# Optimization experiments

Hardware: AMD Instinct MI355X
Metric: run time of the kernel (lower is better)

## Reference

```python
import jax, jax.numpy as jnp
import numpy as np

T, B = 32, 64
H, W = 16, 16
FEAT = 32
CNN_DIM = 512
N_ACT = 5
MAP_OUT = FEAT * H * W  # 8192, flattened map readout


def _conv_relu(x, w, b, stride):
    y = jax.lax.conv_general_dilated(
        x, w, (stride, stride), 'VALID',
        dimension_numbers=('NCHW', 'OIHW', 'NCHW'))
    return jax.nn.relu(y + b[None, :, None, None])


def _mlp(x, w1, b1, w2, b2):
    return jax.nn.relu(x @ w1 + b1) @ w2 + b2


def setup_inputs() -> dict:
    key = jax.random.key(0)
    ks = jax.random.split(key, 32)
    g = lambda k, shape, fan: jax.random.normal(k, shape, jnp.float32) * (1.0 / np.sqrt(fan))
    inp = {}
    inp['image'] = jax.random.uniform(ks[0], (T * B, 84, 84, 3), jnp.float32) * 255.0
    inp['done'] = jnp.zeros((T, B), jnp.float32)
    inp['state0'] = jnp.zeros((B, FEAT, H, W), jnp.float32)
    inp['position'] = jax.random.randint(ks[1], (T * B, 2), 0, H).astype(jnp.int32)
    # NatureCNN params
    inp['w1'] = g(ks[2], (32, 3, 8, 8), 3 * 8 * 8); inp['b1'] = jnp.zeros((32,), jnp.float32)
    inp['w2'] = g(ks[3], (64, 32, 4, 4), 32 * 4 * 4); inp['b2'] = jnp.zeros((64,), jnp.float32)
    inp['w3'] = g(ks[4], (64, 64, 3, 3), 64 * 3 * 3); inp['b3'] = jnp.zeros((64,), jnp.float32)
    inp['wfc'] = g(ks[5], (64 * 7 * 7, CNN_DIM), 64 * 7 * 7); inp['bfc'] = jnp.zeros((CNN_DIM,), jnp.float32)
    # Map write projection
    inp['Ww'] = g(ks[6], (CNN_DIM, FEAT), CNN_DIM); inp['bw'] = jnp.zeros((FEAT,), jnp.float32)
    # pos_net MLP: one-hot(16)+one-hot(16)=32 -> 64
    inp['wp1'] = g(ks[7], (2 * H, 64), 2 * H); inp['bp1'] = jnp.zeros((64,), jnp.float32)
    inp['wp2'] = g(ks[8], (64, 64), 64); inp['bp2'] = jnp.zeros((64,), jnp.float32)
    # policy MLP: (MAP_OUT+64) -> 64 -> N_ACT
    inp['wpo1'] = g(ks[9], (MAP_OUT + 64, 64), MAP_OUT + 64); inp['bpo1'] = jnp.zeros((64,), jnp.float32)
    inp['wpo2'] = g(ks[10], (64, N_ACT), 64) * 0.01; inp['bpo2'] = jnp.zeros((N_ACT,), jnp.float32)
    # value MLP
    inp['wv1'] = g(ks[11], (MAP_OUT + 64, 64), MAP_OUT + 64); inp['bv1'] = jnp.zeros((64,), jnp.float32)
    inp['wv2'] = g(ks[12], (64, 1), 64); inp['bv2'] = jnp.zeros((1,), jnp.float32)
    return inp


def reference(image, done, state0, w1, b1, w2, b2, w3, b3, wfc, bfc, Ww, bw,
              wp1, bp1, wp2, bp2, wpo1, bpo1, wpo2, bpo2, wv1, bv1, wv2, bv2,
              position):
    # preprocess_image: /255 and NHWC -> NCHW
    x = jnp.transpose(image / 255.0, (0, 3, 1, 2))
    x = _conv_relu(x, w1, b1, 4)   # [TB,32,20,20]
    x = _conv_relu(x, w2, b2, 2)   # [TB,64,9,9]
    x = _conv_relu(x, w3, b3, 1)   # [TB,64,7,7]
    h = jax.nn.relu(x.reshape(x.shape[0], -1) @ wfc + bfc)  # [TB,512]

    h_seq = h.reshape(T, B, CNN_DIM)
    idx_seq = position.reshape(T, B, 2)
    benv = jnp.arange(B)

    def step(state, inp):
        h_t, d_t, i_t = inp
        masked = (1.0 - d_t)[:, None, None, None] * state  # reset done envs
        wfeat = h_t @ Ww + bw                              # [B,FEAT]
        state = masked.at[benv, :, i_t[:, 0], i_t[:, 1]].add(wfeat)
        return state, state.reshape(B, -1)                 # per-step map readout

    state, outs = jax.lax.scan(step, state0, (h_seq, done, idx_seq))
    hidden = outs.reshape(T * B, MAP_OUT)

    # position net on one-hot coords
    pos_oh = jnp.concatenate([jax.nn.one_hot(position[:, 0], H, dtype=hidden.dtype),
                              jax.nn.one_hot(position[:, 1], W, dtype=hidden.dtype)], axis=1)
    pos_feat = _mlp(pos_oh, wp1, bp1, wp2, bp2)            # [TB,64]
    hidden = jnp.concatenate([hidden, pos_feat], axis=1)

    logits = _mlp(hidden, wpo1, bpo1, wpo2, bpo2)          # [TB,N_ACT]
    v = _mlp(hidden, wv1, bv1, wv2, bv2)                   # [TB,1]
    return logits, v, state
```

## Files before the change

### kernel.cpp

```cpp
#include <hip/hip_runtime.h>
#include <hip/hip_bf16.h>


#define TT 32
#define BB 64
#define TBR 2048

typedef _Float16 half_t;
typedef __attribute__((ext_vector_type(4))) _Float16 half4;
typedef __attribute__((ext_vector_type(8))) _Float16 half8;
typedef __attribute__((ext_vector_type(4))) float f32x4;

#define OFF_W1T   0u
#define OFF_W2T   6144u
#define OFF_W3T   22528u
#define OFF_WF    40960u
#define OFF_PF    106496u
#define OFF_Y0    237568u
#define OFF_PP    245760u
#define OFF_H     507904u
#define OFF_DELTA 1556480u
#define OFF_WFCT  1818624u
#define OFF_C3    2621440u
#define OFF_H1    5832704u

__global__ __launch_bounds__(256) void prep_all(
    const float* __restrict__ w1, const float* __restrict__ w2,
    const float* __restrict__ w3, half_t* __restrict__ w1p,
    half_t* __restrict__ w2T, half_t* __restrict__ w3T,
    const float* __restrict__ wfc, half_t* __restrict__ wfcT) {
  __shared__ float t[32][33];
  int bx = blockIdx.x;
  if (bx < 304) {
    int g = bx * 256 + threadIdx.x;
    if (g < 8192) {
      int kk = g & 31, oc = (g >> 5) & 31, tap = g >> 10;
      half_t v = (half_t)0.f;
      if (kk < 24) {
        int kx = kk / 3, c = kk - 3 * kx;
        v = (half_t)(w1[oc * 192 + c * 64 + tap * 8 + kx] * (1.0f / 255.0f));
      }
      w1p[g] = v;
      return;
    }
    int g2 = g - 8192;
    if (g2 < 32768) {
      int c = g2 & 31, oc = (g2 >> 5) & 63, tap = g2 >> 11;
      w2T[g2] = (half_t)w2[oc * 512 + c * 16 + tap];
      return;
    }
    int g3 = g2 - 32768;
    if (g3 < 36864) {
      int c = g3 & 63, oc = (g3 >> 6) & 63, tap = g3 >> 12;
      w3T[g3] = (half_t)w3[oc * 576 + c * 9 + tap];
    }
    return;
  }
  int gb = bx - 304;
  int k0 = (gb % 98) * 32, n0 = (gb / 98) * 32;
  int tx = threadIdx.x & 31, ty = threadIdx.x >> 5;
#pragma unroll
  for (int i = 0; i < 4; ++i)
    t[ty + 8 * i][tx] = wfc[(size_t)(k0 + ty + 8 * i) * 512 + n0 + tx];
  __syncthreads();
#pragma unroll
  for (int i = 0; i < 4; ++i)
    wfcT[(size_t)(n0 + ty + 8 * i) * 3136 + k0 + tx] =
        (half_t)t[tx][ty + 8 * i];
}

#define C1_BANDF 5040
#define C1_BANDV 1260
#define C1OUT_OFF 10368
#define C1A(ip, bp)                                                     \
  (C1OUT_OFF + ((ip) >> 1) * 128 +                                      \
   (((((ip) & 1) << 6) | ((bp) & 0x30)) ^ ((((ip) >> 1) & 7) << 4)) +   \
   ((bp) & 15))
#define C2A(ir, bp) \
  ((ir) * 128 + (((bp) & 0x70) ^ (((ir) & 7) << 4)) + ((bp) & 15))
__global__ __launch_bounds__(256) void conv123_mfma(
    const float* __restrict__ img, const half_t* __restrict__ w1p,
    const float* __restrict__ b1, const half_t* __restrict__ w2T,
    const float* __restrict__ b2, const half_t* __restrict__ w3T,
    const float* __restrict__ b3, half_t* __restrict__ out) {
  __shared__ __align__(16) char lds[35968];
  half_t* stag = (half_t*)lds;
  int tid = threadIdx.x;
  int li = blockIdx.x;
  int w = tid >> 6, l = tid & 63, lc = l & 15, q = l >> 4;
  const float* ib = img + (size_t)li * 21168;

  half8 bfrag1[8][2];
#pragma unroll
  for (int tap = 0; tap < 8; ++tap)
#pragma unroll
    for (int t = 0; t < 2; ++t)
      bfrag1[tap][t] =
          *(const half8*)(w1p + (size_t)(tap * 32 + t * 16 + lc) * 32 + q * 8);
  float b1v[2] = {b1[lc], b1[16 + lc]};

  f32x4 fr[5];
#define C1_LOADB(b)                                                   \
  {                                                                   \
    const float* src = ib + 4032 * (b);                               \
    _Pragma("unroll") for (int i = 0; i < 5; ++i) {                   \
      int g = tid + 256 * i;                                          \
      if (g < C1_BANDV) fr[i] = *(const f32x4*)(src + 4 * g);         \
    }                                                                 \
  }
#define C1_WRITEB()                                                   \
  {                                                                   \
    _Pragma("unroll") for (int i = 0; i < 5; ++i) {                   \
      int g = tid + 256 * i;                                          \
      if (g < C1_BANDV) {                                             \
        half4 o;                                                      \
        _Pragma("unroll") for (int j = 0; j < 4; ++j)                 \
            o[j] = (half_t)fr[i][j];                                  \
        *(half4*)&stag[4 * g] = o;                                    \
      }                                                               \
    }                                                                 \
  }

  C1_LOADB(0);
  C1_WRITEB();
  __syncthreads();
  for (int b = 0; b < 5; ++b) {
    if (b < 4) C1_LOADB(b + 1);
    for (int tile = w; tile < 5; tile += 4) {
      int lp = tile * 16 + lc;
      int oyl = lp / 20, ox = lp - oyl * 20;
      f32x4 acc[2];
      acc[0] = (f32x4){0.f, 0.f, 0.f, 0.f};
      acc[1] = (f32x4){0.f, 0.f, 0.f, 0.f};
#pragma unroll
      for (int ky = 0; ky < 8; ++ky) {
        half8 af;
        if (q < 3) {
          const half_t* p = &stag[(4 * oyl + ky) * 252 + 12 * ox + q * 8];
          *(half4*)&af = *(const half4*)p;
          *((half4*)&af + 1) = *((const half4*)(p + 4));
        } else {
#pragma unroll
          for (int j = 0; j < 8; ++j) af[j] = (half_t)0.f;
        }
        acc[0] = __builtin_amdgcn_mfma_f32_16x16x32_f16(af, bfrag1[ky][0],
                                                        acc[0], 0, 0, 0);
        acc[1] = __builtin_amdgcn_mfma_f32_16x16x32_f16(af, bfrag1[ky][1],
                                                        acc[1], 0, 0, 0);
      }
#pragma unroll
      for (int t = 0; t < 2; ++t) {
#pragma unroll
        for (int r = 0; r < 4; ++r) {
          int ip = b * 80 + tile * 16 + q * 4 + r;
          int ch = t * 16 + lc;
          *(half_t*)(lds + C1A(ip, 2 * ch)) =
              (half_t)fmaxf(acc[t][r] + b1v[t], 0.f);
        }
      }
    }
    __syncthreads();
    if (b < 4) {
      C1_WRITEB();
      __syncthreads();
    }
  }

  {
    half8 bfrag2[16][2];
#pragma unroll
    for (int tap = 0; tap < 16; ++tap)
#pragma unroll
      for (int j = 0; j < 2; ++j) {
        int nt = (w & 1) * 2 + j;
        bfrag2[tap][j] = *(const half8*)(
            w2T + (size_t)(tap * 64 + nt * 16 + lc) * 32 + q * 8);
      }
    float b2v[2];
#pragma unroll
    for (int j = 0; j < 2; ++j) b2v[j] = b2[(w & 1) * 32 + j * 16 + lc];

#pragma unroll
    for (int ti = 0; ti < 3; ++ti) {
      int tile = (w >> 1) + 2 * ti;
      int row16 = tile * 16 + lc;
      int orow = row16 < 81 ? row16 : 80;
      int oy = orow / 9, ox = orow - oy * 9;
      f32x4 acc[2];
      acc[0] = (f32x4){0.f, 0.f, 0.f, 0.f};
      acc[1] = (f32x4){0.f, 0.f, 0.f, 0.f};
#pragma unroll
      for (int tap = 0; tap < 16; ++tap) {
        int ky = tap >> 2, kx = tap & 3;
        int ip = (2 * oy + ky) * 20 + 2 * ox + kx;
        half8 af = *(const half8*)(lds + C1A(ip, q * 16));
        acc[0] = __builtin_amdgcn_mfma_f32_16x16x32_f16(af, bfrag2[tap][0],
                                                        acc[0], 0, 0, 0);
        acc[1] = __builtin_amdgcn_mfma_f32_16x16x32_f16(af, bfrag2[tap][1],
                                                        acc[1], 0, 0, 0);
      }
#pragma unroll
      for (int j = 0; j < 2; ++j) {
#pragma unroll
        for (int r = 0; r < 4; ++r) {
          int mr = tile * 16 + q * 4 + r;
          if (mr < 81) {
            int col = (w & 1) * 32 + j * 16 + lc;
            *(half_t*)(lds + C2A(mr, 2 * col)) =
                (half_t)fmaxf(acc[j][r] + b2v[j], 0.f);
          }
        }
      }
    }
  }
  __syncthreads();

  {
    half8 bfrag3[9][2];
#pragma unroll
    for (int tap = 0; tap < 9; ++tap)
#pragma unroll
      for (int ch = 0; ch < 2; ++ch)
        bfrag3[tap][ch] = *(const half8*)(
            w3T + (size_t)(tap * 64 + w * 16 + lc) * 64 + ch * 32 + q * 8);
    float b3v = b3[w * 16 + lc];

    half_t* ob = out + (size_t)li * 3136;
#pragma unroll
    for (int tile = 0; tile < 4; ++tile) {
      int row16 = tile * 16 + lc;
      int orow = row16 < 49 ? row16 : 48;
      int oy = orow / 7, ox = orow - oy * 7;
      f32x4 acc = (f32x4){0.f, 0.f, 0.f, 0.f};
#pragma unroll
      for (int tap = 0; tap < 9; ++tap) {
        int ky = tap / 3, kx = tap - ky * 3;
        int ir = (oy + ky) * 9 + ox + kx;
#pragma unroll
        for (int ch = 0; ch < 2; ++ch) {
          half8 af = *(const half8*)(lds + C2A(ir, ch * 64 + q * 16));
          acc = __builtin_amdgcn_mfma_f32_16x16x32_f16(af, bfrag3[tap][ch],
                                                       acc, 0, 0, 0);
        }
      }
#pragma unroll
      for (int r = 0; r < 4; ++r) {
        int pos = tile * 16 + q * 4 + r;
        if (pos < 49) {
          int col = w * 16 + lc;
          ob[(size_t)col * 49 + pos] = (half_t)fmaxf(acc[r] + b3v, 0.f);
        }
      }
    }
  }
}

__global__ __launch_bounds__(256) void fc_mfma(
    const half_t* __restrict__ A, const half_t* __restrict__ Bt,
    float* __restrict__ h0, float* __restrict__ h1) {
  __shared__ __align__(16) half_t As[2][64 * 40];
  __shared__ __align__(16) half_t Bs[2][64 * 40];
  int tid = threadIdx.x;
  int m0 = blockIdx.y * 64, n0 = blockIdx.x * 64;
  int kh = blockIdx.z;
  int w = tid >> 6;
  int l = tid & 63;
  int lc = l & 15, q = l >> 4;
  int srow = tid >> 2, sseg = tid & 3;

  const half_t* aPtr = A + (size_t)(m0 + srow) * 3136 + kh * 1568 + sseg * 8;
  const half_t* bPtr = Bt + (size_t)(n0 + srow) * 3136 + kh * 1568 + sseg * 8;
  uint4 aReg = *(const uint4*)aPtr;
  uint4 bReg = *(const uint4*)bPtr;

  f32x4 acc[4];
#pragma unroll
  for (int t = 0; t < 4; ++t) acc[t] = (f32x4){0.f, 0.f, 0.f, 0.f};

  for (int s = 0; s < 49; ++s) {
    int cur = s & 1;
    *(uint4*)&As[cur][srow * 40 + sseg * 8] = aReg;
    *(uint4*)&Bs[cur][srow * 40 + sseg * 8] = bReg;
    __syncthreads();
    if (s < 48) {
      aReg = *(const uint4*)(aPtr + (s + 1) * 32);
      bReg = *(const uint4*)(bPtr + (s + 1) * 32);
    }
    half8 af = *(const half8*)&As[cur][(w * 16 + lc) * 40 + q * 8];
#pragma unroll
    for (int t = 0; t < 4; ++t) {
      half8 bf = *(const half8*)&Bs[cur][(t * 16 + lc) * 40 + q * 8];
      acc[t] = __builtin_amdgcn_mfma_f32_16x16x32_f16(af, bf, acc[t], 0, 0, 0);
    }
  }
  float* H = kh ? h1 : h0;
#pragma unroll
  for (int t = 0; t < 4; ++t) {
#pragma unroll
    for (int r = 0; r < 4; ++r) {
      int row = m0 + w * 16 + q * 4 + r;
      int col = n0 + t * 16 + lc;
      H[(size_t)row * 512 + col] = acc[t][r];
    }
  }
}

__global__ __launch_bounds__(256) void mid1_kernel(
    const float* __restrict__ h0, const float* __restrict__ h1,
    const float* __restrict__ bfc, const float* __restrict__ Ww,
    const float* __restrict__ bw, float* __restrict__ wf,
    const int* __restrict__ pos, const float* __restrict__ wp1,
    const float* __restrict__ bp1, const float* __restrict__ wp2,
    const float* __restrict__ bp2, float* __restrict__ pf,
    const float* __restrict__ s0, const float* __restrict__ wpo1,
    const float* __restrict__ wv1, float* __restrict__ y0) {
  __shared__ float red[128];
  int bx = blockIdx.x;
  if (bx < 256) {
    int g = bx * 256 + threadIdx.x;
    int row = g >> 5, oc = g & 31;
    float acc = bw[oc];
    const float* hr0 = h0 + (size_t)row * 512;
    const float* hr1 = h1 + (size_t)row * 512;
#pragma unroll 8
    for (int k = 0; k < 512; ++k)
      acc += fmaxf(hr0[k] + hr1[k] + bfc[k], 0.f) * Ww[k * 32 + oc];
    wf[g] = acc;
    return;
  }
  if (bx < 768) {
    int row = ((bx - 256) * 256 + threadIdx.x) >> 6;
    int l = threadIdx.x & 63;
    int p0 = pos[row * 2], p1 = pos[row * 2 + 1];
    float t1 = fmaxf(wp1[p0 * 64 + l] + wp1[(16 + p1) * 64 + l] + bp1[l], 0.f);
    float acc = bp2[l];
#pragma unroll
    for (int k = 0; k < 64; ++k) acc += __shfl(t1, k) * wp2[k * 64 + l];
    pf[row * 64 + l] = acc;
    return;
  }
  int g = bx - 768;
  int b = g >> 5, kc = g & 31;
  int n = threadIdx.x & 127, kh = threadIdx.x >> 7;
  const float* W = (n < 64) ? (wpo1 + n) : (wv1 + (n - 64));
  int k0 = kc * 256 + kh * 128;
  const float* s = s0 + (size_t)b * 8192 + k0;
  float acc = 0.f;
#pragma unroll 8
  for (int j = 0; j < 128; ++j) acc += s[j] * W[(size_t)(k0 + j) * 64];
  if (kh) red[n] = acc;
  __syncthreads();
  if (!kh) atomicAdd(y0 + b * 128 + n, acc + red[n]);
}

__global__ __launch_bounds__(256) void mid2_kernel(
    const int* __restrict__ pos, const float* __restrict__ wf,
    const float* __restrict__ wpo1, const float* __restrict__ wv1,
    float* __restrict__ delta, const float* __restrict__ s0,
    const float* __restrict__ done, float* __restrict__ out_state,
    const float* __restrict__ pf, float* __restrict__ pp) {
  int bx = blockIdx.x;
  if (bx < 1024) {
    int row = bx * 2 + (threadIdx.x >> 7);
    int n = threadIdx.x & 127;
    const float* W = (n < 64) ? (wpo1 + n) : (wv1 + (n - 64));
    int off = pos[row * 2] * 16 + pos[row * 2 + 1];
    const float* wfr = wf + row * 32;
    float d = 0.f;
#pragma unroll
    for (int c = 0; c < 32; ++c) d += wfr[c] * W[(size_t)(c * 256 + off) * 64];
    delta[(size_t)row * 128 + n] = d;
    return;
  }
  if (bx < 1088) {
    int b = bx - 1024, tid = threadIdx.x;
    float s[32];
#pragma unroll
    for (int c = 0; c < 32; ++c) s[c] = s0[(size_t)b * 8192 + c * 256 + tid];
    for (int t = 0; t < TT; ++t) {
      int row = t * BB + b;
      float mask = 1.f - done[row];
      int off = pos[row * 2] * 16 + pos[row * 2 + 1];
#pragma unroll
      for (int c = 0; c < 32; ++c) s[c] *= mask;
      if (tid == off) {
#pragma unroll
        for (int c = 0; c < 32; ++c) s[c] += wf[row * 32 + c];
      }
    }
#pragma unroll
    for (int c = 0; c < 32; ++c)
      out_state[(size_t)b * 8192 + c * 256 + tid] = s[c];
    return;
  }
  int row = (bx - 1088) * 2 + (threadIdx.x >> 7);
  int n = threadIdx.x & 127;
  const float* W = (n < 64) ? (wpo1 + n) : (wv1 + (n - 64));
  const float* pfr = pf + row * 64;
  float acc = 0.f;
#pragma unroll
  for (int k = 0; k < 64; ++k) acc += pfr[k] * W[(size_t)(8192 + k) * 64];
  pp[(size_t)row * 128 + n] = acc;
}

__global__ __launch_bounds__(128) void scan_head_kernel(
    const float* __restrict__ y0, const float* __restrict__ done,
    const float* __restrict__ delta, const float* __restrict__ pp,
    const float* __restrict__ bpo1, const float* __restrict__ bv1,
    const float* __restrict__ wpo2, const float* __restrict__ bpo2,
    const float* __restrict__ wv2, const float* __restrict__ bv2,
    float* __restrict__ logits, float* __restrict__ vout) {
  int b = blockIdx.x;
  int n = threadIdx.x;
  int l = n & 63, wv = n >> 6;
  float bias1 = wv ? bv1[l] : bpo1[l];
  float w2v[5];
  if (!wv) {
#pragma unroll
    for (int a = 0; a < 5; ++a) w2v[a] = wpo2[l * 5 + a];
  } else {
    w2v[0] = wv2[l];
  }
  float y = y0[b * 128 + n];
  for (int t = 0; t < TT; ++t) {
    int row = t * BB + b;
    y = y * (1.f - done[row]) + delta[(size_t)row * 128 + n];
    float act = fmaxf(y + pp[(size_t)row * 128 + n] + bias1, 0.f);
    if (!wv) {
#pragma unroll
      for (int a = 0; a < 5; ++a) {
        float pa = act * w2v[a];
#pragma unroll
        for (int m = 32; m >= 1; m >>= 1) pa += __shfl_xor(pa, m);
        if (l == 0) logits[row * 5 + a] = pa + bpo2[a];
      }
    } else {
      float pv = act * w2v[0];
#pragma unroll
      for (int m = 32; m >= 1; m >>= 1) pv += __shfl_xor(pv, m);
      if (l == 0) vout[row] = pv + bv2[0];
    }
  }
}

extern "C" void kernel_launch(void* const* d_in, const int* in_sizes, int n_in,
                              void* d_out, int out_size, void* d_ws, size_t ws_size,
                              hipStream_t stream) {
  const float* image = (const float*)d_in[0];
  const float* done = (const float*)d_in[1];
  const float* state0 = (const float*)d_in[2];
  const int* position = (const int*)d_in[3];
  const float* w1 = (const float*)d_in[4];
  const float* b1 = (const float*)d_in[5];
  const float* w2 = (const float*)d_in[6];
  const float* b2 = (const float*)d_in[7];
  const float* w3 = (const float*)d_in[8];
  const float* b3 = (const float*)d_in[9];
  const float* wfc = (const float*)d_in[10];
  const float* bfc = (const float*)d_in[11];
  const float* Ww = (const float*)d_in[12];
  const float* bw = (const float*)d_in[13];
  const float* wp1 = (const float*)d_in[14];
  const float* bp1 = (const float*)d_in[15];
  const float* wp2 = (const float*)d_in[16];
  const float* bp2 = (const float*)d_in[17];
  const float* wpo1 = (const float*)d_in[18];
  const float* bpo1 = (const float*)d_in[19];
  const float* wpo2 = (const float*)d_in[20];
  const float* bpo2 = (const float*)d_in[21];
  const float* wv1 = (const float*)d_in[22];
  const float* bv1 = (const float*)d_in[23];
  const float* wv2 = (const float*)d_in[24];
  const float* bv2 = (const float*)d_in[25];

  float* ws = (float*)d_ws;
  half_t* w1p = (half_t*)(ws + OFF_W1T);
  half_t* w2T = (half_t*)(ws + OFF_W2T);
  half_t* w3T = (half_t*)(ws + OFF_W3T);
  float* wf = ws + OFF_WF;
  float* pfb = ws + OFF_PF;
  float* y0 = ws + OFF_Y0;
  float* ppb = ws + OFF_PP;
  float* h0b = ws + OFF_H;
  float* h1b = ws + OFF_H1;
  float* deltab = ws + OFF_DELTA;
  half_t* wfcT = (half_t*)(ws + OFF_WFCT);
  half_t* c3b = (half_t*)(ws + OFF_C3);

  float* out = (float*)d_out;
  float* out_logits = out;
  float* out_v = out + 10240;
  float* out_state = out + 12288;

  hipMemsetAsync(y0, 0, 8192 * sizeof(float), stream);
  prep_all<<<1872, 256, 0, stream>>>(w1, w2, w3, w1p, w2T, w3T, wfc, wfcT);
  conv123_mfma<<<TBR, 256, 0, stream>>>(image, w1p, b1, w2T, b2, w3T, b3, c3b);
  fc_mfma<<<dim3(8, 32, 2), 256, 0, stream>>>(c3b, wfcT, h0b, h1b);
  mid1_kernel<<<2816, 256, 0, stream>>>(h0b, h1b, bfc, Ww, bw, wf, position,
                                        wp1, bp1, wp2, bp2, pfb, state0,
                                        wpo1, wv1, y0);
  mid2_kernel<<<2112, 256, 0, stream>>>(position, wf, wpo1, wv1, deltab,
                                        state0, done, out_state, pfb, ppb);
  scan_head_kernel<<<64, 128, 0, stream>>>(y0, done, deltab, ppb, bpo1, bv1,
                                           wpo2, bpo2, wv2, bv2,
                                           out_logits, out_v);
}
```

Baseline: 451.8 us.

## Enlarge FC GEMM tiles to 128x128 and split K four ways

The FC MFMA GEMM now computes 128x128 output tiles per block, with each wave holding a 2x8 grid of 16x16 accumulators, up from 64x64. The K dimension is split into four chunks instead of two, giving 256 blocks, and mid1 sums four partial outputs. The larger tiles raise operand reuse from LDS and cut global reloads of A and B. In exchange the blocks use more registers and LDS, and two extra partial buffers must be written and read back.

New measurement: 449.8 us. No clear change (-0.4%).

```diff
diff --git a/kernel.cpp b/kernel.cpp
--- a/kernel.cpp
+++ b/kernel.cpp
@@ -23,6 +23,8 @@
 #define OFF_WFCT  1818624u
 #define OFF_C3    2621440u
 #define OFF_H1    5832704u
+#define OFF_H2    6881280u
+#define OFF_H3    7929856u
 
 __global__ __launch_bounds__(256) void prep_all(
     const float* __restrict__ w1, const float* __restrict__ w2,
@@ -245,10 +247,10 @@
       }
 #pragma unroll
       for (int r = 0; r < 4; ++r) {
-        int pos = tile * 16 + q * 4 + r;
-        if (pos < 49) {
+        int pos2 = tile * 16 + q * 4 + r;
+        if (pos2 < 49) {
           int col = w * 16 + lc;
-          ob[(size_t)col * 49 + pos] = (half_t)fmaxf(acc[r] + b3v, 0.f);
+          ob[(size_t)col * 49 + pos2] = (half_t)fmaxf(acc[r] + b3v, 0.f);
         }
       }
     }
@@ -257,56 +259,77 @@
 
 __global__ __launch_bounds__(256) void fc_mfma(
     const half_t* __restrict__ A, const half_t* __restrict__ Bt,
-    float* __restrict__ h0, float* __restrict__ h1) {
-  __shared__ __align__(16) half_t As[2][64 * 40];
-  __shared__ __align__(16) half_t Bs[2][64 * 40];
+    float* __restrict__ h0, float* __restrict__ h1,
+    float* __restrict__ h2, float* __restrict__ h3) {
+  __shared__ __align__(16) half_t As[2][128 * 40];
+  __shared__ __align__(16) half_t Bs[2][128 * 40];
   int tid = threadIdx.x;
-  int m0 = blockIdx.y * 64, n0 = blockIdx.x * 64;
-  int kh = blockIdx.z;
+  int n0 = blockIdx.x * 128, m0 = blockIdx.y * 128;
+  int kc = blockIdx.z;
+  const int kofs[4] = {0, 800, 1600, 2368};
+  const int kstp[4] = {25, 25, 24, 24};
+  int k0 = kofs[kc], NS = kstp[kc];
   int w = tid >> 6;
   int l = tid & 63;
   int lc = l & 15, q = l >> 4;
   int srow = tid >> 2, sseg = tid & 3;
 
-  const half_t* aPtr = A + (size_t)(m0 + srow) * 3136 + kh * 1568 + sseg * 8;
-  const half_t* bPtr = Bt + (size_t)(n0 + srow) * 3136 + kh * 1568 + sseg * 8;
-  uint4 aReg = *(const uint4*)aPtr;
-  uint4 bReg = *(const uint4*)bPtr;
-
-  f32x4 acc[4];
-#pragma unroll
-  for (int t = 0; t < 4; ++t) acc[t] = (f32x4){0.f, 0.f, 0.f, 0.f};
-
-  for (int s = 0; s < 49; ++s) {
+  const half_t* aP0 = A + (size_t)(m0 + srow) * 3136 + k0 + sseg * 8;
+  const half_t* aP1 = A + (size_t)(m0 + srow + 64) * 3136 + k0 + sseg * 8;
+  const half_t* bP0 = Bt + (size_t)(n0 + srow) * 3136 + k0 + sseg * 8;
+  const half_t* bP1 = Bt + (size_t)(n0 + srow + 64) * 3136 + k0 + sseg * 8;
+  uint4 aR0 = *(const uint4*)aP0, aR1 = *(const uint4*)aP1;
+  uint4 bR0 = *(const uint4*)bP0, bR1 = *(const uint4*)bP1;
+
+  f32x4 acc[2][8];
+#pragma unroll
+  for (int m = 0; m < 2; ++m)
+#pragma unroll
+    for (int t = 0; t < 8; ++t) acc[m][t] = (f32x4){0.f, 0.f, 0.f, 0.f};
+
+  for (int s = 0; s < NS; ++s) {
     int cur = s & 1;
-    *(uint4*)&As[cur][srow * 40 + sseg * 8] = aReg;
-    *(uint4*)&Bs[cur][srow * 40 + sseg * 8] = bReg;
+    *(uint4*)&As[cur][srow * 40 + sseg * 8] = aR0;
+    *(uint4*)&As[cur][(srow + 64) * 40 + sseg * 8] = aR1;
+    *(uint4*)&Bs[cur][srow * 40 + sseg * 8] = bR0;
+    *(uint4*)&Bs[cur][(srow + 64) * 40 + sseg * 8] = bR1;
     __syncthreads();
-    if (s < 48) {
-      aReg = *(const uint4*)(aPtr + (s + 1) * 32);
-      bReg = *(const uint4*)(bPtr + (s + 1) * 32);
-    }
-    half8 af = *(const half8*)&As[cur][(w * 16 + lc) * 40 + q * 8];
-#pragma unroll
-    for (int t = 0; t < 4; ++t) {
+    if (s + 1 < NS) {
+      int o = (s + 1) * 32;
+      aR0 = *(const uint4*)(aP0 + o);
+      aR1 = *(const uint4*)(aP1 + o);
+      bR0 = *(const uint4*)(bP0 + o);
+      bR1 = *(const uint4*)(bP1 + o);
+    }
+    half8 af[2];
+#pragma unroll
+    for (int m = 0; m < 2; ++m)
+      af[m] = *(const half8*)&As[cur][(w * 32 + m * 16 + lc) * 40 + q * 8];
+#pragma unroll
+    for (int t = 0; t < 8; ++t) {
       half8 bf = *(const half8*)&Bs[cur][(t * 16 + lc) * 40 + q * 8];
-      acc[t] = __builtin_amdgcn_mfma_f32_16x16x32_f16(af, bf, acc[t], 0, 0, 0);
-    }
-  }
-  float* H = kh ? h1 : h0;
-#pragma unroll
-  for (int t = 0; t < 4; ++t) {
-#pragma unroll
-    for (int r = 0; r < 4; ++r) {
-      int row = m0 + w * 16 + q * 4 + r;
-      int col = n0 + t * 16 + lc;
-      H[(size_t)row * 512 + col] = acc[t][r];
-    }
-  }
+      acc[0][t] = __builtin_amdgcn_mfma_f32_16x16x32_f16(af[0], bf,
+                                                         acc[0][t], 0, 0, 0);
+      acc[1][t] = __builtin_amdgcn_mfma_f32_16x16x32_f16(af[1], bf,
+                                                         acc[1][t], 0, 0, 0);
+    }
+  }
+  float* H = (kc == 0) ? h0 : (kc == 1) ? h1 : (kc == 2) ? h2 : h3;
+#pragma unroll
+  for (int m = 0; m < 2; ++m)
+#pragma unroll
+    for (int t = 0; t < 8; ++t)
+#pragma unroll
+      for (int r = 0; r < 4; ++r) {
+        int row = m0 + w * 32 + m * 16 + q * 4 + r;
+        int col = n0 + t * 16 + lc;
+        H[(size_t)row * 512 + col] = acc[m][t][r];
+      }
 }
 
 __global__ __launch_bounds__(256) void mid1_kernel(
     const float* __restrict__ h0, const float* __restrict__ h1,
+    const float* __restrict__ h2, const float* __restrict__ h3,
     const float* __restrict__ bfc, const float* __restrict__ Ww,
     const float* __restrict__ bw, float* __restrict__ wf,
     const int* __restrict__ pos, const float* __restrict__ wp1,
@@ -322,9 +345,12 @@
     float acc = bw[oc];
     const float* hr0 = h0 + (size_t)row * 512;
     const float* hr1 = h1 + (size_t)row * 512;
+    const float* hr2 = h2 + (size_t)row * 512;
+    const float* hr3 = h3 + (size_t)row * 512;
 #pragma unroll 8
     for (int k = 0; k < 512; ++k)
-      acc += fmaxf(hr0[k] + hr1[k] + bfc[k], 0.f) * Ww[k * 32 + oc];
+      acc += fmaxf(hr0[k] + hr1[k] + hr2[k] + hr3[k] + bfc[k], 0.f) *
+             Ww[k * 32 + oc];
     wf[g] = acc;
     return;
   }
@@ -483,6 +509,8 @@
   float* ppb = ws + OFF_PP;
   float* h0b = ws + OFF_H;
   float* h1b = ws + OFF_H1;
+  float* h2b = ws + OFF_H2;
+  float* h3b = ws + OFF_H3;
   float* deltab = ws + OFF_DELTA;
   half_t* wfcT = (half_t*)(ws + OFF_WFCT);
   half_t* c3b = (half_t*)(ws + OFF_C3);
@@ -495,10 +523,10 @@
   hipMemsetAsync(y0, 0, 8192 * sizeof(float), stream);
   prep_all<<<1872, 256, 0, stream>>>(w1, w2, w3, w1p, w2T, w3T, wfc, wfcT);
   conv123_mfma<<<TBR, 256, 0, stream>>>(image, w1p, b1, w2T, b2, w3T, b3, c3b);
-  fc_mfma<<<dim3(8, 32, 2), 256, 0, stream>>>(c3b, wfcT, h0b, h1b);
-  mid1_kernel<<<2816, 256, 0, stream>>>(h0b, h1b, bfc, Ww, bw, wf, position,
-                                        wp1, bp1, wp2, bp2, pfb, state0,
-                                        wpo1, wv1, y0);
+  fc_mfma<<<dim3(4, 16, 4), 256, 0, stream>>>(c3b, wfcT, h0b, h1b, h2b, h3b);
+  mid1_kernel<<<2816, 256, 0, stream>>>(h0b, h1b, h2b, h3b, bfc, Ww, bw, wf,
+                                        position, wp1, bp1, wp2, bp2, pfb,
+                                        state0, wpo1, wv1, y0);
   mid2_kernel<<<2112, 256, 0, stream>>>(position, wf, wpo1, wv1, deltab,
                                         state0, done, out_state, pfb, ppb);
   scan_head_kernel<<<64, 128, 0, stream>>>(y0, done, deltab, ppb, bpo1, bv1,
```
